# Optimization experiments

Hardware: AMD Instinct MI355X
Metric: run time of the kernel (lower is better)

Reference implementation:

```python
import jax, jax.numpy as jnp
import numpy as np

B, L, Q, K, H = 64, 1024, 1024, 1024, 1024

def setup_inputs() -> dict:
    key = jax.random.key(0)
    k1, k2, k3, k4, k5, k6 = jax.random.split(key, 6)
    query = jax.random.normal(k1, (B, Q), dtype=jnp.float32)
    keys = jax.random.normal(k2, (B, L, K), dtype=jnp.float32)
    mask = jax.random.randint(k3, (B, L), 0, 2).astype(bool)
    # nn.Linear weights: W1 [H, Q], W2 [H, K], v [1, H], all bias-free
    W1 = jax.random.normal(k4, (H, Q), dtype=jnp.float32) / np.sqrt(Q)
    W2 = jax.random.normal(k5, (H, K), dtype=jnp.float32) / np.sqrt(K)
    v = jax.random.normal(k6, (1, H), dtype=jnp.float32) / np.sqrt(H)
    return {"query": query, "keys": keys, "mask": mask, "W1": W1, "W2": W2, "v": v}

def reference(query, keys, mask, W1, W2, v):
    # q: [B, H], broadcast over seq dim instead of expand
    q = query @ W1.T                                  # [B, H]
    k = jnp.einsum('blk,hk->blh', keys, W2)           # [B, L, H]
    scores = jnp.tanh(q[:, None, :] + k) @ v[0]       # [B, L]
    scores = jnp.where(mask, -jnp.inf, scores)
    weights = jax.nn.softmax(scores, axis=-1)
    weights = jnp.nan_to_num(weights, nan=0.0)
    context = jnp.einsum('bl,blk->bk', weights, keys) # [B, K]
    return (context, weights)
```

## Files before the change

kernel.cpp:

```cpp
#include <hip/hip_runtime.h>
#include <math.h>


typedef __attribute__((ext_vector_type(8))) short short8;
typedef __attribute__((ext_vector_type(4))) float floatx4;

__device__ __forceinline__ short f2bf(float x) {
    unsigned u = __float_as_uint(x);
    u += 0x7fffu + ((u >> 16) & 1u);
    return (short)(u >> 16);
}
__device__ __forceinline__ short8 pack8(float4 lo, float4 hi) {
    short8 r;
    r[0]=f2bf(lo.x); r[1]=f2bf(lo.y); r[2]=f2bf(lo.z); r[3]=f2bf(lo.w);
    r[4]=f2bf(hi.x); r[5]=f2bf(hi.y); r[6]=f2bf(hi.z); r[7]=f2bf(hi.w);
    return r;
}

#define LDA 40

__global__ __launch_bounds__(256) void k0_zero(float* __restrict__ out) {
    const int i = (blockIdx.x * 256 + threadIdx.x) * 4;
    const float4 z = {0.f, 0.f, 0.f, 0.f};
    *(float4*)(out + i) = z;
}

__global__ __launch_bounds__(256) void k1_qproj(
    const float* __restrict__ query, const float* __restrict__ W1,
    float* __restrict__ out)
{
    __shared__ float As[32][64];
    __shared__ float Bs[32][64];
    const int t  = threadIdx.x;
    const int tx = t & 15, ty = t >> 4;
    const int h0 = blockIdx.x * 64;
    const int kbase = blockIdx.y * 256;
    const int sr = t >> 2;
    const int sk = (t & 3) * 8;
    float c[4][4] = {{0.f}};
    for (int k0 = kbase; k0 < kbase + 256; k0 += 32) {
        const float4 a0 = *(const float4*)(query + sr * 1024 + k0 + sk);
        const float4 a1 = *(const float4*)(query + sr * 1024 + k0 + sk + 4);
        const float4 b0 = *(const float4*)(W1 + (h0 + sr) * 1024 + k0 + sk);
        const float4 b1 = *(const float4*)(W1 + (h0 + sr) * 1024 + k0 + sk + 4);
        __syncthreads();
        As[sk+0][sr]=a0.x; As[sk+1][sr]=a0.y; As[sk+2][sr]=a0.z; As[sk+3][sr]=a0.w;
        As[sk+4][sr]=a1.x; As[sk+5][sr]=a1.y; As[sk+6][sr]=a1.z; As[sk+7][sr]=a1.w;
        Bs[sk+0][sr]=b0.x; Bs[sk+1][sr]=b0.y; Bs[sk+2][sr]=b0.z; Bs[sk+3][sr]=b0.w;
        Bs[sk+4][sr]=b1.x; Bs[sk+5][sr]=b1.y; Bs[sk+6][sr]=b1.z; Bs[sk+7][sr]=b1.w;
        __syncthreads();
        #pragma unroll
        for (int k = 0; k < 32; ++k) {
            const float4 av = *(const float4*)&As[k][ty*4];
            const float4 bv = *(const float4*)&Bs[k][tx*4];
            const float aa[4] = {av.x, av.y, av.z, av.w};
            const float bb[4] = {bv.x, bv.y, bv.z, bv.w};
            #pragma unroll
            for (int i = 0; i < 4; ++i)
                #pragma unroll
                for (int j = 0; j < 4; ++j)
                    c[i][j] = fmaf(aa[i], bb[j], c[i][j]);
        }
    }
    #pragma unroll
    for (int i = 0; i < 4; ++i)
        #pragma unroll
        for (int j = 0; j < 4; ++j)
            atomicAdd(&out[(ty*4 + i) * 1024 + h0 + tx*4 + j], c[i][j]);
}

__global__ __launch_bounds__(256) void k2_scores(
    const float* __restrict__ keys, const float* __restrict__ W2,
    const float* __restrict__ v, float* __restrict__ out)
{
    __shared__ union {
        struct { short A[128][LDA]; short B[128][LDA]; } st;
        float red[128][33];
    } sm;
    const int t  = threadIdx.x;
    const int hb = blockIdx.x;
    const int l0 = blockIdx.y * 128;
    const int b  = blockIdx.z;
    const int h0 = hb * 128;
    const float* q = out;
    float* score = out + 65536;

    const int srow = t >> 1;
    const int skh  = (t & 1) * 16;
    const float* Arow = keys + ((size_t)(b * 1024 + l0 + srow)) * 1024 + skh;
    const float* Brow = W2   + ((size_t)(h0 + srow)) * 1024 + skh;

    const int lane = t & 63, wid = t >> 6;
    const int quad = lane >> 4, m16 = lane & 15;
    const int wm = (wid >> 1) * 64;
    const int wn = (wid & 1) * 64;

    floatx4 acc[4][4] = {};

    for (int kk = 0; kk < 1024; kk += 32) {
        const float4 a0 = *(const float4*)(Arow + kk);
        const float4 a1 = *(const float4*)(Arow + kk + 4);
        const float4 a2 = *(const float4*)(Arow + kk + 8);
        const float4 a3 = *(const float4*)(Arow + kk + 12);
        const float4 w0 = *(const float4*)(Brow + kk);
        const float4 w1 = *(const float4*)(Brow + kk + 4);
        const float4 w2 = *(const float4*)(Brow + kk + 8);
        const float4 w3 = *(const float4*)(Brow + kk + 12);
        __syncthreads();
        *(short8*)&sm.st.A[srow][skh]     = pack8(a0, a1);
        *(short8*)&sm.st.A[srow][skh + 8] = pack8(a2, a3);
        *(short8*)&sm.st.B[srow][skh]     = pack8(w0, w1);
        *(short8*)&sm.st.B[srow][skh + 8] = pack8(w2, w3);
        __syncthreads();
        short8 af[4], bf[4];
        #pragma unroll
        for (int i = 0; i < 4; ++i)
            af[i] = *(const short8*)&sm.st.A[wm + i*16 + m16][quad * 8];
        #pragma unroll
        for (int j = 0; j < 4; ++j)
            bf[j] = *(const short8*)&sm.st.B[wn + j*16 + m16][quad * 8];
        #pragma unroll
        for (int i = 0; i < 4; ++i)
            #pragma unroll
            for (int j = 0; j < 4; ++j)
                acc[i][j] = __builtin_amdgcn_mfma_f32_16x16x32_bf16(af[i], bf[j], acc[i][j], 0, 0, 0);
    }

    float qv[4], vv[4];
    #pragma unroll
    for (int j = 0; j < 4; ++j) {
        const int h = h0 + wn + j * 16 + m16;
        qv[j] = q[b * 1024 + h];
        vv[j] = v[h];
    }
    __syncthreads();
    #pragma unroll
    for (int i = 0; i < 4; ++i) {
        #pragma unroll
        for (int r = 0; r < 4; ++r) {
            float s = 0.f;
            #pragma unroll
            for (int j = 0; j < 4; ++j)
                s += tanhf(qv[j] + acc[i][j][r]) * vv[j];
            sm.red[wm + i * 16 + quad * 4 + r][(wid & 1) * 16 + m16] = s;
        }
    }
    __syncthreads();
    if (t < 128) {
        const float* rr = sm.red[t];
        float s = 0.f;
        #pragma unroll
        for (int c = 0; c < 32; ++c) s += rr[c];
        atomicAdd(&score[b * 1024 + l0 + t], s);
    }
}

__global__ __launch_bounds__(256) void k3_softmax(
    const unsigned char* __restrict__ mask_u8, float* __restrict__ out)
{
    __shared__ float sc[1024];
    __shared__ float red[256];
    __shared__ int nz_sh;
    const int b = blockIdx.x;
    const int t = threadIdx.x;

    if (t == 0) nz_sh = 0;
    __syncthreads();
    {
        int nz = 0;
        #pragma unroll
        for (int j = 1; j < 4; ++j)
            if (mask_u8[t * 4 + j] != 0) nz = 1;
        if (nz) atomicAdd(&nz_sh, 1);
    }
    __syncthreads();
    const int use_i32 = (nz_sh == 0);
    const int* mask_i32 = (const int*)mask_u8;

    float* score = out + 65536;
    float lmax = -INFINITY;
    #pragma unroll
    for (int i = 0; i < 4; ++i) {
        const int l = t + i * 256;
        float s = score[b * 1024 + l];
        const int ml = b * 1024 + l;
        const bool masked = use_i32 ? (mask_i32[ml] != 0) : (mask_u8[ml] != 0);
        if (masked) s = -INFINITY;
        sc[l] = s;
        lmax = fmaxf(lmax, s);
    }
    red[t] = lmax;
    __syncthreads();
    for (int off = 128; off > 0; off >>= 1) {
        if (t < off) red[t] = fmaxf(red[t], red[t + off]);
        __syncthreads();
    }
    const float m = red[0];
    __syncthreads();
    float e[4];
    float lsum = 0.f;
    #pragma unroll
    for (int i = 0; i < 4; ++i) {
        const float s = sc[t + i * 256];
        const float ev = (s > -INFINITY && m > -INFINITY) ? expf(s - m) : 0.f;
        e[i] = ev;
        lsum += ev;
    }
    red[t] = lsum;
    __syncthreads();
    for (int off = 128; off > 0; off >>= 1) {
        if (t < off) red[t] += red[t + off];
        __syncthreads();
    }
    const float S = red[0];
    const float inv = (S > 0.f) ? (1.f / S) : 0.f;
    #pragma unroll
    for (int i = 0; i < 4; ++i)
        score[b * 1024 + t + i * 256] = e[i] * inv;
    const float4 z = {0.f, 0.f, 0.f, 0.f};
    ((float4*)(out + b * 1024))[t] = z;
}

__global__ __launch_bounds__(256) void k4_context(
    const float* __restrict__ keys, float* __restrict__ out)
{
    __shared__ float w[128];
    const int t  = threadIdx.x;
    const int b  = blockIdx.y;
    const int l0 = blockIdx.x * 128;
    if (t < 128) w[t] = out[65536 + b * 1024 + l0 + t];
    __syncthreads();
    const float4* kp = (const float4*)(keys + ((size_t)b * 1024 + (size_t)l0) * 1024) + t;
    float4 acc = {0.f, 0.f, 0.f, 0.f};
    #pragma unroll 4
    for (int l = 0; l < 128; ++l) {
        const float4 kv = kp[(size_t)l * 256];
        const float wv = w[l];
        acc.x = fmaf(wv, kv.x, acc.x);
        acc.y = fmaf(wv, kv.y, acc.y);
        acc.z = fmaf(wv, kv.z, acc.z);
        acc.w = fmaf(wv, kv.w, acc.w);
    }
    float* o = out + b * 1024 + t * 4;
    atomicAdd(o + 0, acc.x);
    atomicAdd(o + 1, acc.y);
    atomicAdd(o + 2, acc.z);
    atomicAdd(o + 3, acc.w);
}

extern "C" void kernel_launch(void* const* d_in, const int* in_sizes, int n_in,
                              void* d_out, int out_size, void* d_ws, size_t ws_size,
                              hipStream_t stream) {
    const float*         query = (const float*)d_in[0];
    const float*         keys  = (const float*)d_in[1];
    const unsigned char* mask  = (const unsigned char*)d_in[2];
    const float*         W1    = (const float*)d_in[3];
    const float*         W2    = (const float*)d_in[4];
    const float*         v     = (const float*)d_in[5];
    float* out = (float*)d_out;
    (void)d_ws; (void)ws_size;

    k0_zero   <<<dim3(128),       256, 0, stream>>>(out);
    k1_qproj  <<<dim3(16, 4),     256, 0, stream>>>(query, W1, out);
    k2_scores <<<dim3(8, 8, 64),  256, 0, stream>>>(keys, W2, v, out);
    k3_softmax<<<dim3(64),        256, 0, stream>>>(mask, out);
    k4_context<<<dim3(8, 64),     256, 0, stream>>>(keys, out);
}
```

Measured before the change: 790.0 us.

## Pre-convert W2 to bf16, swizzle LDS tiles, reorder blocks, drop context atomics

```diff
diff --git a/kernel.cpp b/kernel.cpp
--- a/kernel.cpp
+++ b/kernel.cpp
@@ -4,25 +4,28 @@
 
 typedef __attribute__((ext_vector_type(8))) short short8;
 typedef __attribute__((ext_vector_type(4))) float floatx4;
-
-__device__ __forceinline__ short f2bf(float x) {
-    unsigned u = __float_as_uint(x);
-    u += 0x7fffu + ((u >> 16) & 1u);
-    return (short)(u >> 16);
-}
-__device__ __forceinline__ short8 pack8(float4 lo, float4 hi) {
-    short8 r;
-    r[0]=f2bf(lo.x); r[1]=f2bf(lo.y); r[2]=f2bf(lo.z); r[3]=f2bf(lo.w);
-    r[4]=f2bf(hi.x); r[5]=f2bf(hi.y); r[6]=f2bf(hi.z); r[7]=f2bf(hi.w);
-    return r;
-}
-
-#define LDA 40
+typedef __attribute__((ext_vector_type(8))) float float8v;
+typedef __attribute__((ext_vector_type(8))) __bf16 bf16x8;
+
+__device__ __forceinline__ short8 cvt8(float4 lo, float4 hi) {
+    float8v f = {lo.x, lo.y, lo.z, lo.w, hi.x, hi.y, hi.z, hi.w};
+    bf16x8 b = __builtin_convertvector(f, bf16x8);
+    union { bf16x8 b; short8 s; } u; u.b = b;
+    return u.s;
+}
 
 __global__ __launch_bounds__(256) void k0_zero(float* __restrict__ out) {
     const int i = (blockIdx.x * 256 + threadIdx.x) * 4;
     const float4 z = {0.f, 0.f, 0.f, 0.f};
     *(float4*)(out + i) = z;
+}
+
+__global__ __launch_bounds__(256) void kconv_w2(const float* __restrict__ W2,
+                                                unsigned short* __restrict__ W2b) {
+    const int i = (blockIdx.x * 256 + threadIdx.x) * 8;
+    const float4 lo = *(const float4*)(W2 + i);
+    const float4 hi = *(const float4*)(W2 + i + 4);
+    *(short8*)(W2b + i) = cvt8(lo, hi);
 }
 
 __global__ __launch_bounds__(256) void k1_qproj(
@@ -71,29 +74,39 @@
 
 __global__ __launch_bounds__(256) void k2_scores(
     const float* __restrict__ keys, const float* __restrict__ W2,
-    const float* __restrict__ v, float* __restrict__ out)
+    const unsigned short* __restrict__ W2b, const float* __restrict__ v,
+    float* __restrict__ out, int w2bf)
 {
     __shared__ union {
-        struct { short A[128][LDA]; short B[128][LDA]; } st;
+        struct { short A[128][32]; short B[128][32]; } st;
         float red[128][33];
     } sm;
     const int t  = threadIdx.x;
-    const int hb = blockIdx.x;
-    const int l0 = blockIdx.y * 128;
-    const int b  = blockIdx.z;
+    const int id = blockIdx.x;
+    const int lt = id & 7;
+    const int n  = id >> 3;
+    const int hb = n & 7;
+    const int b  = n >> 3;
+    const int l0 = lt * 128;
     const int h0 = hb * 128;
     const float* q = out;
     float* score = out + 65536;
 
-    const int srow = t >> 1;
-    const int skh  = (t & 1) * 16;
-    const float* Arow = keys + ((size_t)(b * 1024 + l0 + srow)) * 1024 + skh;
-    const float* Brow = W2   + ((size_t)(h0 + srow)) * 1024 + skh;
+    const int r  = t >> 1;
+    const int ch = (t & 1) * 2;
+    const int xr = (r >> 1) & 3;
+    const int p0 = (ch    ) ^ xr;
+    const int p1 = (ch + 1) ^ xr;
+    const float*          Arow = keys + ((size_t)(b * 1024 + l0 + r)) * 1024 + ch * 8;
+    const float*          Bfrow = W2  + ((size_t)(h0 + r)) * 1024 + ch * 8;
+    const unsigned short* Bbrow = W2b + ((size_t)(h0 + r)) * 1024 + ch * 8;
 
     const int lane = t & 63, wid = t >> 6;
     const int quad = lane >> 4, m16 = lane & 15;
     const int wm = (wid >> 1) * 64;
     const int wn = (wid & 1) * 64;
+    const int xf = (m16 >> 1) & 3;
+    const int pa = quad ^ xf;
 
     floatx4 acc[4][4] = {};
 
@@ -102,23 +115,31 @@
         const float4 a1 = *(const float4*)(Arow + kk + 4);
         const float4 a2 = *(const float4*)(Arow + kk + 8);
         const float4 a3 = *(const float4*)(Arow + kk + 12);
-        const float4 w0 = *(const float4*)(Brow + kk);
-        const float4 w1 = *(const float4*)(Brow + kk + 4);
-        const float4 w2 = *(const float4*)(Brow + kk + 8);
-        const float4 w3 = *(const float4*)(Brow + kk + 12);
-        __syncthreads();
-        *(short8*)&sm.st.A[srow][skh]     = pack8(a0, a1);
-        *(short8*)&sm.st.A[srow][skh + 8] = pack8(a2, a3);
-        *(short8*)&sm.st.B[srow][skh]     = pack8(w0, w1);
-        *(short8*)&sm.st.B[srow][skh + 8] = pack8(w2, w3);
+        short8 bs0, bs1;
+        if (w2bf) {
+            bs0 = *(const short8*)(Bbrow + kk);
+            bs1 = *(const short8*)(Bbrow + kk + 8);
+        } else {
+            const float4 w0 = *(const float4*)(Bfrow + kk);
+            const float4 w1 = *(const float4*)(Bfrow + kk + 4);
+            const float4 w2_ = *(const float4*)(Bfrow + kk + 8);
+            const float4 w3 = *(const float4*)(Bfrow + kk + 12);
+            bs0 = cvt8(w0, w1);
+            bs1 = cvt8(w2_, w3);
+        }
+        __syncthreads();
+        *(short8*)&sm.st.A[r][p0 * 8] = cvt8(a0, a1);
+        *(short8*)&sm.st.A[r][p1 * 8] = cvt8(a2, a3);
+        *(short8*)&sm.st.B[r][p0 * 8] = bs0;
+        *(short8*)&sm.st.B[r][p1 * 8] = bs1;
         __syncthreads();
         short8 af[4], bf[4];
         #pragma unroll
         for (int i = 0; i < 4; ++i)
-            af[i] = *(const short8*)&sm.st.A[wm + i*16 + m16][quad * 8];
+            af[i] = *(const short8*)&sm.st.A[wm + i*16 + m16][pa * 8];
         #pragma unroll
         for (int j = 0; j < 4; ++j)
-            bf[j] = *(const short8*)&sm.st.B[wn + j*16 + m16][quad * 8];
+            bf[j] = *(const short8*)&sm.st.B[wn + j*16 + m16][pa * 8];
         #pragma unroll
         for (int i = 0; i < 4; ++i)
             #pragma unroll
@@ -137,20 +158,20 @@
     #pragma unroll
     for (int i = 0; i < 4; ++i) {
         #pragma unroll
-        for (int r = 0; r < 4; ++r) {
+        for (int rr = 0; rr < 4; ++rr) {
             float s = 0.f;
             #pragma unroll
             for (int j = 0; j < 4; ++j)
-                s += tanhf(qv[j] + acc[i][j][r]) * vv[j];
-            sm.red[wm + i * 16 + quad * 4 + r][(wid & 1) * 16 + m16] = s;
+                s += tanhf(qv[j] + acc[i][j][rr]) * vv[j];
+            sm.red[wm + i * 16 + quad * 4 + rr][(wid & 1) * 16 + m16] = s;
         }
     }
     __syncthreads();
     if (t < 128) {
-        const float* rr = sm.red[t];
+        const float* rw = sm.red[t];
         float s = 0.f;
         #pragma unroll
-        for (int c = 0; c < 32; ++c) s += rr[c];
+        for (int c = 0; c < 32; ++c) s += rw[c];
         atomicAdd(&score[b * 1024 + l0 + t], s);
     }
 }
@@ -224,16 +245,21 @@
 __global__ __launch_bounds__(256) void k4_context(
     const float* __restrict__ keys, float* __restrict__ out)
 {
-    __shared__ float w[128];
+    __shared__ float w[1024];
+    __shared__ float4 part[8][32];
     const int t  = threadIdx.x;
+    const int kc = blockIdx.x;
     const int b  = blockIdx.y;
-    const int l0 = blockIdx.x * 128;
-    if (t < 128) w[t] = out[65536 + b * 1024 + l0 + t];
-    __syncthreads();
-    const float4* kp = (const float4*)(keys + ((size_t)b * 1024 + (size_t)l0) * 1024) + t;
+    #pragma unroll
+    for (int i = 0; i < 4; ++i)
+        w[t + i * 256] = out[65536 + b * 1024 + t + i * 256];
+    __syncthreads();
+    const int r8 = t >> 5;
+    const int c4 = t & 31;
+    const float4* kp = (const float4*)(keys + (size_t)b * 1048576) + kc * 32 + c4;
     float4 acc = {0.f, 0.f, 0.f, 0.f};
-    #pragma unroll 4
-    for (int l = 0; l < 128; ++l) {
+    #pragma unroll 8
+    for (int l = r8; l < 1024; l += 8) {
         const float4 kv = kp[(size_t)l * 256];
         const float wv = w[l];
         acc.x = fmaf(wv, kv.x, acc.x);
@@ -241,11 +267,17 @@
         acc.z = fmaf(wv, kv.z, acc.z);
         acc.w = fmaf(wv, kv.w, acc.w);
     }
-    float* o = out + b * 1024 + t * 4;
-    atomicAdd(o + 0, acc.x);
-    atomicAdd(o + 1, acc.y);
-    atomicAdd(o + 2, acc.z);
-    atomicAdd(o + 3, acc.w);
+    part[r8][c4] = acc;
+    __syncthreads();
+    if (t < 32) {
+        float4 s = part[0][t];
+        #pragma unroll
+        for (int rr = 1; rr < 8; ++rr) {
+            const float4 pv = part[rr][t];
+            s.x += pv.x; s.y += pv.y; s.z += pv.z; s.w += pv.w;
+        }
+        *(float4*)(out + b * 1024 + kc * 128 + t * 4) = s;
+    }
 }
 
 extern "C" void kernel_launch(void* const* d_in, const int* in_sizes, int n_in,
@@ -258,11 +290,16 @@
     const float*         W2    = (const float*)d_in[4];
     const float*         v     = (const float*)d_in[5];
     float* out = (float*)d_out;
-    (void)d_ws; (void)ws_size;
-
-    k0_zero   <<<dim3(128),       256, 0, stream>>>(out);
-    k1_qproj  <<<dim3(16, 4),     256, 0, stream>>>(query, W1, out);
-    k2_scores <<<dim3(8, 8, 64),  256, 0, stream>>>(keys, W2, v, out);
-    k3_softmax<<<dim3(64),        256, 0, stream>>>(mask, out);
-    k4_context<<<dim3(8, 64),     256, 0, stream>>>(keys, out);
-}
+
+    const bool  w2ws = (ws_size >= (size_t)(2 * 1024 * 1024 + 64));
+    unsigned short* W2b = (unsigned short*)d_ws;
+
+    k0_zero   <<<dim3(128),     256, 0, stream>>>(out);
+    if (w2ws)
+        kconv_w2<<<dim3(512),   256, 0, stream>>>(W2, W2b);
+    k1_qproj  <<<dim3(16, 4),   256, 0, stream>>>(query, W1, out);
+    k2_scores <<<dim3(4096),    256, 0, stream>>>(keys, W2, w2ws ? W2b : (unsigned short*)nullptr,
+                                                  v, out, w2ws ? 1 : 0);
+    k3_softmax<<<dim3(64),      256, 0, stream>>>(mask, out);
+    k4_context<<<dim3(8, 64),   256, 0, stream>>>(keys, out);
+}
```

Result: slower. 834.7 us (+5.7%).
